# Kernel optimization log

Hardware: AMD Instinct MI355X
Metric: run time of the kernel (lower is better)

The kernel has to match this reference:

```python
import jax, jax.numpy as jnp
import numpy as np

N = 50000          # nodes
E = 800000         # edges (avg degree 16)
IN_C = 3
HEADS = 4
NUM_GRAPHS = 8
NUM_CLASSES = 10


def setup_inputs() -> dict:
    key = jax.random.key(0)
    ks = jax.random.split(key, 12)
    x = jax.random.normal(ks[0], (N, IN_C), jnp.float32)
    edge_index = jax.random.randint(ks[1], (2, E), 0, N, dtype=jnp.int64)
    batch = jnp.sort(jax.random.randint(ks[2], (N,), 0, NUM_GRAPHS, dtype=jnp.int64))

    def glorot(k, shape, fan):
        return jax.random.normal(k, shape, jnp.float32) * np.float32(1.0 / np.sqrt(fan))

    return {
        "x": x, "edge_index": edge_index, "batch": batch,
        "fc0_w": glorot(ks[3], (IN_C, 16), IN_C), "fc0_b": jnp.zeros((16,), jnp.float32),
        "u1": glorot(ks[4], (16, HEADS), 16), "c1": jnp.zeros((HEADS,), jnp.float32),
        "w1": glorot(ks[5], (16, HEADS * 32), 16), "b1": jnp.zeros((32,), jnp.float32),
        "u2": glorot(ks[6], (32, HEADS), 32), "c2": jnp.zeros((HEADS,), jnp.float32),
        "w2": glorot(ks[7], (32, HEADS * 64), 32), "b2": jnp.zeros((64,), jnp.float32),
        "fc1_w": glorot(ks[8], (64, NUM_CLASSES), 64), "fc1_b": jnp.zeros((NUM_CLASSES,), jnp.float32),
    }


def feast_conv(x, src, dst, u, c, w, b, heads, out_c):
    """FeaStConv (t_inv=True): per-edge head softmax on (x_j - x_i), mean aggregation."""
    n = x.shape[0]
    # soft-assignment over heads: [E, H]
    q = jax.nn.softmax((x[src] - x[dst]) @ u + c, axis=-1)
    # transform at node level, then gather per edge: [E, H, out_c]
    xw = (x @ w).reshape(n, heads, out_c)
    msg = jnp.einsum('eh,ehc->ec', q, xw[src])           # [E, out_c]
    agg = jax.ops.segment_sum(msg, dst, num_segments=n)  # sum over incoming edges
    cnt = jax.ops.segment_sum(jnp.ones((src.shape[0],), x.dtype), dst, num_segments=n)
    return agg / jnp.maximum(cnt, 1.0)[:, None] + b


def global_mean_pool(x, batch, num_graphs):
    s = jax.ops.segment_sum(x, batch, num_segments=num_graphs)
    cnt = jax.ops.segment_sum(jnp.ones((x.shape[0],), x.dtype), batch, num_segments=num_graphs)
    return s / jnp.maximum(cnt, 1.0)[:, None]


def reference(x, edge_index, batch, fc0_w, fc0_b, u1, c1, w1, b1, u2, c2, w2, b2, fc1_w, fc1_b):
    src, dst = edge_index[0], edge_index[1]   # x_j = x[src], x_i = x[dst]
    h = jax.nn.relu(x @ fc0_w + fc0_b)                              # [N, 16]
    h = jax.nn.relu(feast_conv(h, src, dst, u1, c1, w1, b1, HEADS, 32))  # [N, 32]
    h = jax.nn.relu(feast_conv(h, src, dst, u2, c2, w2, b2, HEADS, 64))  # [N, 64]
    g = global_mean_pool(h, batch, NUM_GRAPHS)                      # [G, 64]
    # dropout is identity in eval mode
    return g @ fc1_w + fc1_b                                        # [G, num_classes]
```

## Files before the change

### kernel.cpp

```cpp
#include <hip/hip_runtime.h>

#define N_NODES 50000
#define N_EDGES 800000
#define HEADS 4
#define NUM_GRAPHS 8

__global__ __launch_bounds__(256) void hist_kernel(const int* __restrict__ dst,
                                                   int* __restrict__ deg,
                                                   int* __restrict__ off) {
  int e = blockIdx.x * blockDim.x + threadIdx.x;
  if (e < N_EDGES) off[e] = atomicAdd(&deg[dst[e]], 1);
}

__global__ __launch_bounds__(256) void alloc_kernel(const int* __restrict__ deg,
                                                    int* __restrict__ gctr,
                                                    int* __restrict__ rowstart) {
  int i = blockIdx.x * blockDim.x + threadIdx.x;
  int lane = threadIdx.x & 63;
  int d = (i < N_NODES) ? deg[i] : 0;
  int pre = d;
#pragma unroll
  for (int offd = 1; offd < 64; offd <<= 1) {
    int v = __shfl_up(pre, offd, 64);
    if (lane >= offd) pre += v;
  }
  int total = __shfl(pre, 63, 64);
  int base = 0;
  if (lane == 63) base = atomicAdd(gctr, total);
  base = __shfl(base, 63, 64);
  if (i < N_NODES) rowstart[i] = base + pre - d;
}

__global__ __launch_bounds__(256) void scatter_kernel(const int* __restrict__ src,
                                                      const int* __restrict__ dst,
                                                      const int* __restrict__ rowstart,
                                                      const int* __restrict__ off,
                                                      int* __restrict__ src_perm) {
  int e = blockIdx.x * blockDim.x + threadIdx.x;
  if (e >= N_EDGES) return;
  int p = rowstart[dst[e]] + off[e];
  src_perm[p] = src[e];
}

__global__ __launch_bounds__(256) void fc0_kernel(
    const float* __restrict__ x,
    const float* __restrict__ fc0_w, const float* __restrict__ fc0_b,
    const float* __restrict__ u1,
    float* __restrict__ h0, float* __restrict__ P1) {
  __shared__ float sW0[3 * 16];
  __shared__ float sB0[16];
  __shared__ float sU[16 * 4];
  for (int i = threadIdx.x; i < 48; i += blockDim.x) sW0[i] = fc0_w[i];
  for (int i = threadIdx.x; i < 16; i += blockDim.x) sB0[i] = fc0_b[i];
  for (int i = threadIdx.x; i < 64; i += blockDim.x) sU[i] = u1[i];
  __syncthreads();
  int n = blockIdx.x * blockDim.x + threadIdx.x;
  if (n >= N_NODES) return;
  float x0 = x[n * 3 + 0], x1 = x[n * 3 + 1], x2 = x[n * 3 + 2];
  float h[16];
#pragma unroll
  for (int j = 0; j < 16; j++) {
    float v = x0 * sW0[0 * 16 + j] + x1 * sW0[1 * 16 + j] + x2 * sW0[2 * 16 + j] + sB0[j];
    h[j] = fmaxf(v, 0.f);
    h0[(size_t)n * 16 + j] = h[j];
  }
  float p0 = 0.f, p1 = 0.f, p2 = 0.f, p3 = 0.f;
#pragma unroll
  for (int j = 0; j < 16; j++) {
    p0 += h[j] * sU[j * 4 + 0];
    p1 += h[j] * sU[j * 4 + 1];
    p2 += h[j] * sU[j * 4 + 2];
    p3 += h[j] * sU[j * 4 + 3];
  }
  reinterpret_cast<float4*>(P1)[n] = make_float4(p0, p1, p2, p3);
}

__global__ __launch_bounds__(256) void proj2_kernel(
    const float* __restrict__ h1, const float* __restrict__ u2,
    float* __restrict__ P2) {
  __shared__ float sU[32 * 4];
  for (int i = threadIdx.x; i < 128; i += blockDim.x) sU[i] = u2[i];
  __syncthreads();
  int n = blockIdx.x * blockDim.x + threadIdx.x;
  if (n >= N_NODES) return;
  const float4* hr = reinterpret_cast<const float4*>(h1 + (size_t)n * 32);
  float p0 = 0.f, p1 = 0.f, p2 = 0.f, p3 = 0.f;
#pragma unroll
  for (int j4 = 0; j4 < 8; j4++) {
    float4 a = hr[j4];
#pragma unroll
    for (int k = 0; k < 4; k++) {
      float hv = k == 0 ? a.x : k == 1 ? a.y : k == 2 ? a.z : a.w;
      int j = 4 * j4 + k;
      p0 += hv * sU[j * 4 + 0];
      p1 += hv * sU[j * 4 + 1];
      p2 += hv * sU[j * 4 + 2];
      p3 += hv * sU[j * 4 + 3];
    }
  }
  reinterpret_cast<float4*>(P2)[n] = make_float4(p0, p1, p2, p3);
}

__global__ __launch_bounds__(256) void q_kernel(
    const int* __restrict__ rowstart, const int* __restrict__ deg,
    const int* __restrict__ src_perm,
    const float* __restrict__ P, const float* __restrict__ cb,
    float* __restrict__ q_perm) {
  int wid = (blockIdx.x * (blockDim.x >> 6)) + (threadIdx.x >> 6);
  int lane = threadIdx.x & 63;
  if (wid >= N_NODES) return;
  float4 Pd = reinterpret_cast<const float4*>(P)[wid];
  float b0 = cb[0] - Pd.x, b1 = cb[1] - Pd.y, b2 = cb[2] - Pd.z, b3 = cb[3] - Pd.w;
  int e0 = rowstart[wid];
  int d = deg[wid];
  for (int l = lane; l < d; l += 64) {
    int p = e0 + l;
    int s = src_perm[p];
    float4 Ps = reinterpret_cast<const float4*>(P)[s];
    float l0 = Ps.x + b0, l1 = Ps.y + b1, l2 = Ps.z + b2, l3 = Ps.w + b3;
    float m = fmaxf(fmaxf(l0, l1), fmaxf(l2, l3));
    float e0v = __expf(l0 - m), e1v = __expf(l1 - m), e2v = __expf(l2 - m), e3v = __expf(l3 - m);
    float inv = 1.f / (e0v + e1v + e2v + e3v);
    reinterpret_cast<float4*>(q_perm)[p] =
        make_float4(e0v * inv, e1v * inv, e2v * inv, e3v * inv);
  }
}

__global__ __launch_bounds__(256) void agg1_kernel(
    const int* __restrict__ rowstart, const int* __restrict__ deg,
    const int* __restrict__ src_perm, const float* __restrict__ q_perm,
    const float* __restrict__ h0,
    float* __restrict__ A) {
  int wave = threadIdx.x >> 6;
  int lane = threadIdx.x & 63;
  int g = lane >> 4;
  int j = lane & 15;
  int node = blockIdx.x * 4 + wave;
  if (node >= N_NODES) return;
  int e0 = rowstart[node];
  int e1 = e0 + deg[node];
  const float4* q4 = reinterpret_cast<const float4*>(q_perm);
  float a0 = 0.f, a1 = 0.f, a2 = 0.f, a3 = 0.f;
  int p = e0;
  for (; p + 16 <= e1; p += 16) {
    int sA = src_perm[p + 0 + g];
    int sB = src_perm[p + 4 + g];
    int sC = src_perm[p + 8 + g];
    int sD = src_perm[p + 12 + g];
    float4 qA = q4[p + 0 + g];
    float4 qB = q4[p + 4 + g];
    float4 qC = q4[p + 8 + g];
    float4 qD = q4[p + 12 + g];
    float fA = h0[(size_t)sA * 16 + j];
    float fB = h0[(size_t)sB * 16 + j];
    float fC = h0[(size_t)sC * 16 + j];
    float fD = h0[(size_t)sD * 16 + j];
    a0 += qA.x * fA + qB.x * fB + qC.x * fC + qD.x * fD;
    a1 += qA.y * fA + qB.y * fB + qC.y * fC + qD.y * fD;
    a2 += qA.z * fA + qB.z * fB + qC.z * fC + qD.z * fD;
    a3 += qA.w * fA + qB.w * fB + qC.w * fC + qD.w * fD;
  }
  for (; p + 4 <= e1; p += 4) {
    int s = src_perm[p + g];
    float4 q = q4[p + g];
    float f = h0[(size_t)s * 16 + j];
    a0 += q.x * f; a1 += q.y * f; a2 += q.z * f; a3 += q.w * f;
  }
  int rem = e1 - p;
  if (g < rem) {
    int s = src_perm[p + g];
    float4 q = q4[p + g];
    float f = h0[(size_t)s * 16 + j];
    a0 += q.x * f; a1 += q.y * f; a2 += q.z * f; a3 += q.w * f;
  }
  a0 += __shfl_xor(a0, 16, 64); a0 += __shfl_xor(a0, 32, 64);
  a1 += __shfl_xor(a1, 16, 64); a1 += __shfl_xor(a1, 32, 64);
  a2 += __shfl_xor(a2, 16, 64); a2 += __shfl_xor(a2, 32, 64);
  a3 += __shfl_xor(a3, 16, 64); a3 += __shfl_xor(a3, 32, 64);
  float o = (g == 0) ? a0 : (g == 1) ? a1 : (g == 2) ? a2 : a3;
  A[(size_t)node * 64 + lane] = o;
}

__global__ __launch_bounds__(256) void agg2_kernel(
    const int* __restrict__ rowstart, const int* __restrict__ deg,
    const int* __restrict__ src_perm, const float* __restrict__ q_perm,
    const float* __restrict__ h1,
    float* __restrict__ A) {
  int wave = threadIdx.x >> 6;
  int lane = threadIdx.x & 63;
  int g = lane >> 5;
  int j = lane & 31;
  int node = blockIdx.x * 4 + wave;
  if (node >= N_NODES) return;
  int e0 = rowstart[node];
  int e1 = e0 + deg[node];
  const float4* q4 = reinterpret_cast<const float4*>(q_perm);
  float a0 = 0.f, a1 = 0.f, a2 = 0.f, a3 = 0.f;
  int p = e0;
  for (; p + 8 <= e1; p += 8) {
    int sA = src_perm[p + 0 + g];
    int sB = src_perm[p + 2 + g];
    int sC = src_perm[p + 4 + g];
    int sD = src_perm[p + 6 + g];
    float4 qA = q4[p + 0 + g];
    float4 qB = q4[p + 2 + g];
    float4 qC = q4[p + 4 + g];
    float4 qD = q4[p + 6 + g];
    float fA = h1[(size_t)sA * 32 + j];
    float fB = h1[(size_t)sB * 32 + j];
    float fC = h1[(size_t)sC * 32 + j];
    float fD = h1[(size_t)sD * 32 + j];
    a0 += qA.x * fA + qB.x * fB + qC.x * fC + qD.x * fD;
    a1 += qA.y * fA + qB.y * fB + qC.y * fC + qD.y * fD;
    a2 += qA.z * fA + qB.z * fB + qC.z * fC + qD.z * fD;
    a3 += qA.w * fA + qB.w * fB + qC.w * fC + qD.w * fD;
  }
  for (; p + 2 <= e1; p += 2) {
    int s = src_perm[p + g];
    float4 q = q4[p + g];
    float f = h1[(size_t)s * 32 + j];
    a0 += q.x * f; a1 += q.y * f; a2 += q.z * f; a3 += q.w * f;
  }
  int rem = e1 - p;
  if (g < rem) {
    int s = src_perm[p + g];
    float4 q = q4[p + g];
    float f = h1[(size_t)s * 32 + j];
    a0 += q.x * f; a1 += q.y * f; a2 += q.z * f; a3 += q.w * f;
  }
  a0 += __shfl_xor(a0, 32, 64);
  a1 += __shfl_xor(a1, 32, 64);
  a2 += __shfl_xor(a2, 32, 64);
  a3 += __shfl_xor(a3, 32, 64);
  float oa = (g == 0) ? a0 : a1;
  float ob = (g == 0) ? a2 : a3;
  A[(size_t)node * 128 + lane] = oa;
  A[(size_t)node * 128 + 64 + lane] = ob;
}

__global__ __launch_bounds__(256) void gemm1_kernel(
    const int* __restrict__ deg, const float* __restrict__ A,
    const float* __restrict__ w1, const float* __restrict__ b1,
    float* __restrict__ h1) {
  __shared__ float sB[64 * 32];
  for (int i = threadIdx.x; i < 64 * 32; i += 256) {
    int hj = i / 32, c = i % 32;
    sB[i] = w1[(hj % 16) * 128 + (hj / 16) * 32 + c];
  }
  __syncthreads();
  const float4* sB4 = reinterpret_cast<const float4*>(sB);
  int c4 = threadIdx.x & 7;
  int g = threadIdx.x >> 3;
  int n0 = blockIdx.x * 64 + g * 2;
  int n1 = n0 + 1;
  int na = min(n0, N_NODES - 1);
  int nb = min(n1, N_NODES - 1);
  const float4* A0 = reinterpret_cast<const float4*>(A + (size_t)na * 64);
  const float4* A1 = reinterpret_cast<const float4*>(A + (size_t)nb * 64);
  float4 bc = reinterpret_cast<const float4*>(b1)[c4];
  float4 acc0 = {0, 0, 0, 0}, acc1 = {0, 0, 0, 0};
#pragma unroll 2
  for (int k4 = 0; k4 < 16; k4++) {
    float4 a0 = A0[k4];
    float4 a1 = A1[k4];
    float4 w0 = sB4[(4 * k4 + 0) * 8 + c4];
    float4 wv1 = sB4[(4 * k4 + 1) * 8 + c4];
    float4 w2v = sB4[(4 * k4 + 2) * 8 + c4];
    float4 w3 = sB4[(4 * k4 + 3) * 8 + c4];
    acc0.x += a0.x * w0.x + a0.y * wv1.x + a0.z * w2v.x + a0.w * w3.x;
    acc0.y += a0.x * w0.y + a0.y * wv1.y + a0.z * w2v.y + a0.w * w3.y;
    acc0.z += a0.x * w0.z + a0.y * wv1.z + a0.z * w2v.z + a0.w * w3.z;
    acc0.w += a0.x * w0.w + a0.y * wv1.w + a0.z * w2v.w + a0.w * w3.w;
    acc1.x += a1.x * w0.x + a1.y * wv1.x + a1.z * w2v.x + a1.w * w3.x;
    acc1.y += a1.x * w0.y + a1.y * wv1.y + a1.z * w2v.y + a1.w * w3.y;
    acc1.z += a1.x * w0.z + a1.y * wv1.z + a1.z * w2v.z + a1.w * w3.z;
    acc1.w += a1.x * w0.w + a1.y * wv1.w + a1.z * w2v.w + a1.w * w3.w;
  }
  if (n0 < N_NODES) {
    float inv = 1.f / fmaxf((float)deg[n0], 1.f);
    float4 o = {fmaxf(acc0.x * inv + bc.x, 0.f), fmaxf(acc0.y * inv + bc.y, 0.f),
                fmaxf(acc0.z * inv + bc.z, 0.f), fmaxf(acc0.w * inv + bc.w, 0.f)};
    reinterpret_cast<float4*>(h1 + (size_t)n0 * 32)[c4] = o;
  }
  if (n1 < N_NODES) {
    float inv = 1.f / fmaxf((float)deg[n1], 1.f);
    float4 o = {fmaxf(acc1.x * inv + bc.x, 0.f), fmaxf(acc1.y * inv + bc.y, 0.f),
                fmaxf(acc1.z * inv + bc.z, 0.f), fmaxf(acc1.w * inv + bc.w, 0.f)};
    reinterpret_cast<float4*>(h1 + (size_t)n1 * 32)[c4] = o;
  }
}

__global__ __launch_bounds__(256) void gemm2_kernel(
    const int* __restrict__ deg, const float* __restrict__ A,
    const float* __restrict__ w2, const float* __restrict__ b2,
    float* __restrict__ h2) {
  __shared__ float sB[128 * 64];
  for (int i = threadIdx.x; i < 128 * 64; i += 256) {
    int hj = i / 64, c = i % 64;
    sB[i] = w2[(hj % 32) * 256 + (hj / 32) * 64 + c];
  }
  __syncthreads();
  const float4* sB4 = reinterpret_cast<const float4*>(sB);
  int c4 = threadIdx.x & 15;
  int g = threadIdx.x >> 4;
  int n0 = blockIdx.x * 32 + g * 2;
  int n1 = n0 + 1;
  int na = min(n0, N_NODES - 1);
  int nb = min(n1, N_NODES - 1);
  const float4* A0 = reinterpret_cast<const float4*>(A + (size_t)na * 128);
  const float4* A1 = reinterpret_cast<const float4*>(A + (size_t)nb * 128);
  float4 bc = reinterpret_cast<const float4*>(b2)[c4];
  float4 acc0 = {0, 0, 0, 0}, acc1 = {0, 0, 0, 0};
#pragma unroll 2
  for (int k4 = 0; k4 < 32; k4++) {
    float4 a0 = A0[k4];
    float4 a1 = A1[k4];
    float4 w0 = sB4[(4 * k4 + 0) * 16 + c4];
    float4 wv1 = sB4[(4 * k4 + 1) * 16 + c4];
    float4 w2v = sB4[(4 * k4 + 2) * 16 + c4];
    float4 w3 = sB4[(4 * k4 + 3) * 16 + c4];
    acc0.x += a0.x * w0.x + a0.y * wv1.x + a0.z * w2v.x + a0.w * w3.x;
    acc0.y += a0.x * w0.y + a0.y * wv1.y + a0.z * w2v.y + a0.w * w3.y;
    acc0.z += a0.x * w0.z + a0.y * wv1.z + a0.z * w2v.z + a0.w * w3.z;
    acc0.w += a0.x * w0.w + a0.y * wv1.w + a0.z * w2v.w + a0.w * w3.w;
    acc1.x += a1.x * w0.x + a1.y * wv1.x + a1.z * w2v.x + a1.w * w3.x;
    acc1.y += a1.x * w0.y + a1.y * wv1.y + a1.z * w2v.y + a1.w * w3.y;
    acc1.z += a1.x * w0.z + a1.y * wv1.z + a1.z * w2v.z + a1.w * w3.z;
    acc1.w += a1.x * w0.w + a1.y * wv1.w + a1.z * w2v.w + a1.w * w3.w;
  }
  if (n0 < N_NODES) {
    float inv = 1.f / fmaxf((float)deg[n0], 1.f);
    float4 o = {fmaxf(acc0.x * inv + bc.x, 0.f), fmaxf(acc0.y * inv + bc.y, 0.f),
                fmaxf(acc0.z * inv + bc.z, 0.f), fmaxf(acc0.w * inv + bc.w, 0.f)};
    reinterpret_cast<float4*>(h2 + (size_t)n0 * 64)[c4] = o;
  }
  if (n1 < N_NODES) {
    float inv = 1.f / fmaxf((float)deg[n1], 1.f);
    float4 o = {fmaxf(acc1.x * inv + bc.x, 0.f), fmaxf(acc1.y * inv + bc.y, 0.f),
                fmaxf(acc1.z * inv + bc.z, 0.f), fmaxf(acc1.w * inv + bc.w, 0.f)};
    reinterpret_cast<float4*>(h2 + (size_t)n1 * 64)[c4] = o;
  }
}

#define POOL_CHUNK 64
__global__ __launch_bounds__(256) void pool_kernel(
    const float* __restrict__ h2, const int* __restrict__ batch,
    float* __restrict__ gsum, float* __restrict__ gcnt) {
  int grp = threadIdx.x / 64;
  int c = threadIdx.x % 64;
  int n0 = (blockIdx.x * 4 + grp) * POOL_CHUNK;
  int n1 = min(n0 + POOL_CHUNK, N_NODES);
  if (n0 >= N_NODES) return;
  float acc = 0.f;
  float cacc = 0.f;
  int curg = batch[n0];
  for (int n = n0; n < n1; n++) {
    int g = batch[n];
    float v = h2[(size_t)n * 64 + c];
    if (g != curg) {
      atomicAdd(&gsum[curg * 64 + c], acc);
      if (c == 0) atomicAdd(&gcnt[curg], cacc);
      acc = 0.f;
      cacc = 0.f;
      curg = g;
    }
    acc += v;
    cacc += 1.f;
  }
  atomicAdd(&gsum[curg * 64 + c], acc);
  if (c == 0) atomicAdd(&gcnt[curg], cacc);
}

__global__ __launch_bounds__(128) void head_kernel(
    const float* __restrict__ gsum, const float* __restrict__ gcnt,
    const float* __restrict__ fc1_w, const float* __restrict__ fc1_b,
    float* __restrict__ out) {
  int t = threadIdx.x;
  if (t >= NUM_GRAPHS * 10) return;
  int g = t / 10, k = t % 10;
  float inv = 1.f / fmaxf(gcnt[g], 1.f);
  float s = fc1_b[k];
#pragma unroll
  for (int c = 0; c < 64; c++) s += gsum[g * 64 + c] * inv * fc1_w[c * 10 + k];
  out[g * 10 + k] = s;
}

extern "C" void kernel_launch(void* const* d_in, const int* in_sizes, int n_in,
                              void* d_out, int out_size, void* d_ws, size_t ws_size,
                              hipStream_t stream) {
  const float* x = (const float*)d_in[0];
  const int* edge_index = (const int*)d_in[1];
  const int* batch = (const int*)d_in[2];
  const float* fc0_w = (const float*)d_in[3];
  const float* fc0_b = (const float*)d_in[4];
  const float* u1 = (const float*)d_in[5];
  const float* c1 = (const float*)d_in[6];
  const float* w1 = (const float*)d_in[7];
  const float* b1 = (const float*)d_in[8];
  const float* u2 = (const float*)d_in[9];
  const float* c2 = (const float*)d_in[10];
  const float* w2 = (const float*)d_in[11];
  const float* b2 = (const float*)d_in[12];
  const float* fc1_w = (const float*)d_in[13];
  const float* fc1_b = (const float*)d_in[14];
  float* out = (float*)d_out;

  const int* src = edge_index;
  const int* dst = edge_index + N_EDGES;

  char* wsb = (char*)d_ws;
  int* deg = (int*)wsb;
  int* gctr = deg + N_NODES;
  int* rowstart = (int*)wsb + 50004;
  int* off = rowstart + N_NODES;
  int* src_perm = off + N_EDGES;
  float* q_perm = (float*)wsb + 1700004;
  float* h0 = q_perm + (size_t)N_EDGES * 4;
  float* h1 = h0 + (size_t)N_NODES * 16;
  float* h2 = h1 + (size_t)N_NODES * 32;
  float* A = h2 + (size_t)N_NODES * 64;
  float* P1 = A + (size_t)N_NODES * 128;
  float* P2 = P1 + (size_t)N_NODES * 4;
  float* gsum = P2 + (size_t)N_NODES * 4;
  float* gcnt = gsum + NUM_GRAPHS * 64;

  hipMemsetAsync(deg, 0, (N_NODES + 1) * sizeof(int), stream);
  hipMemsetAsync(gsum, 0, (NUM_GRAPHS * 64 + NUM_GRAPHS) * sizeof(float), stream);

  int nblk = (N_NODES + 255) / 256;
  int eblk = (N_EDGES + 255) / 256;
  int wblk = (N_NODES + 3) / 4;

  hist_kernel<<<eblk, 256, 0, stream>>>(dst, deg, off);
  alloc_kernel<<<nblk, 256, 0, stream>>>(deg, gctr, rowstart);
  scatter_kernel<<<eblk, 256, 0, stream>>>(src, dst, rowstart, off, src_perm);

  fc0_kernel<<<nblk, 256, 0, stream>>>(x, fc0_w, fc0_b, u1, h0, P1);

  q_kernel<<<wblk, 256, 0, stream>>>(rowstart, deg, src_perm, P1, c1, q_perm);
  agg1_kernel<<<wblk, 256, 0, stream>>>(rowstart, deg, src_perm, q_perm, h0, A);
  gemm1_kernel<<<(N_NODES + 63) / 64, 256, 0, stream>>>(deg, A, w1, b1, h1);

  proj2_kernel<<<nblk, 256, 0, stream>>>(h1, u2, P2);
  q_kernel<<<wblk, 256, 0, stream>>>(rowstart, deg, src_perm, P2, c2, q_perm);
  agg2_kernel<<<wblk, 256, 0, stream>>>(rowstart, deg, src_perm, q_perm, h1, A);
  gemm2_kernel<<<(N_NODES + 31) / 32, 256, 0, stream>>>(deg, A, w2, b2, h2);

  int pblk = (N_NODES + POOL_CHUNK * 4 - 1) / (POOL_CHUNK * 4);
  pool_kernel<<<pblk, 256, 0, stream>>>(h2, batch, gsum, gcnt);
  head_kernel<<<1, 128, 0, stream>>>(gsum, gcnt, fc1_w, fc1_b, out);
}
```

Measured before the change: 301.8 us.

## Flatten q_kernel to per-edge threads, fuse proj2 into gemm1, merge memsets

The scatter now stores (src,dst) pairs so q_kernel can run one thread per edge instead of one wave per node. That removes lane idling on low-degree nodes, where a 64-lane wave covers only about 16 edges. The proj2 kernel is folded into gemm1's epilogue, which computes P2 from the fresh h1 tile and reduces it with shuffles. The two memsets become one by moving gsum/gcnt next to deg. The cost is doubling the index array bandwidth in the agg kernels (int2 loads reading only .x) and an extra random P[dst] gather per edge.

Measured after the change: 281.7 us. 6.7% less time.

```diff
diff --git a/kernel.cpp b/kernel.cpp
--- a/kernel.cpp
+++ b/kernel.cpp
@@ -35,11 +35,12 @@
                                                       const int* __restrict__ dst,
                                                       const int* __restrict__ rowstart,
                                                       const int* __restrict__ off,
-                                                      int* __restrict__ src_perm) {
+                                                      int2* __restrict__ sd) {
   int e = blockIdx.x * blockDim.x + threadIdx.x;
   if (e >= N_EDGES) return;
-  int p = rowstart[dst[e]] + off[e];
-  src_perm[p] = src[e];
+  int d = dst[e];
+  int p = rowstart[d] + off[e];
+  sd[p] = make_int2(src[e], d);
 }
 
 __global__ __launch_bounds__(256) void fc0_kernel(
@@ -75,60 +76,29 @@
   reinterpret_cast<float4*>(P1)[n] = make_float4(p0, p1, p2, p3);
 }
 
-__global__ __launch_bounds__(256) void proj2_kernel(
-    const float* __restrict__ h1, const float* __restrict__ u2,
-    float* __restrict__ P2) {
-  __shared__ float sU[32 * 4];
-  for (int i = threadIdx.x; i < 128; i += blockDim.x) sU[i] = u2[i];
-  __syncthreads();
-  int n = blockIdx.x * blockDim.x + threadIdx.x;
-  if (n >= N_NODES) return;
-  const float4* hr = reinterpret_cast<const float4*>(h1 + (size_t)n * 32);
-  float p0 = 0.f, p1 = 0.f, p2 = 0.f, p3 = 0.f;
-#pragma unroll
-  for (int j4 = 0; j4 < 8; j4++) {
-    float4 a = hr[j4];
-#pragma unroll
-    for (int k = 0; k < 4; k++) {
-      float hv = k == 0 ? a.x : k == 1 ? a.y : k == 2 ? a.z : a.w;
-      int j = 4 * j4 + k;
-      p0 += hv * sU[j * 4 + 0];
-      p1 += hv * sU[j * 4 + 1];
-      p2 += hv * sU[j * 4 + 2];
-      p3 += hv * sU[j * 4 + 3];
-    }
-  }
-  reinterpret_cast<float4*>(P2)[n] = make_float4(p0, p1, p2, p3);
-}
-
 __global__ __launch_bounds__(256) void q_kernel(
-    const int* __restrict__ rowstart, const int* __restrict__ deg,
-    const int* __restrict__ src_perm,
+    const int2* __restrict__ sd,
     const float* __restrict__ P, const float* __restrict__ cb,
     float* __restrict__ q_perm) {
-  int wid = (blockIdx.x * (blockDim.x >> 6)) + (threadIdx.x >> 6);
-  int lane = threadIdx.x & 63;
-  if (wid >= N_NODES) return;
-  float4 Pd = reinterpret_cast<const float4*>(P)[wid];
-  float b0 = cb[0] - Pd.x, b1 = cb[1] - Pd.y, b2 = cb[2] - Pd.z, b3 = cb[3] - Pd.w;
-  int e0 = rowstart[wid];
-  int d = deg[wid];
-  for (int l = lane; l < d; l += 64) {
-    int p = e0 + l;
-    int s = src_perm[p];
-    float4 Ps = reinterpret_cast<const float4*>(P)[s];
-    float l0 = Ps.x + b0, l1 = Ps.y + b1, l2 = Ps.z + b2, l3 = Ps.w + b3;
-    float m = fmaxf(fmaxf(l0, l1), fmaxf(l2, l3));
-    float e0v = __expf(l0 - m), e1v = __expf(l1 - m), e2v = __expf(l2 - m), e3v = __expf(l3 - m);
-    float inv = 1.f / (e0v + e1v + e2v + e3v);
-    reinterpret_cast<float4*>(q_perm)[p] =
-        make_float4(e0v * inv, e1v * inv, e2v * inv, e3v * inv);
-  }
+  int p = blockIdx.x * blockDim.x + threadIdx.x;
+  if (p >= N_EDGES) return;
+  int2 e = sd[p];
+  float4 Ps = reinterpret_cast<const float4*>(P)[e.x];
+  float4 Pd = reinterpret_cast<const float4*>(P)[e.y];
+  float l0 = Ps.x - Pd.x + cb[0];
+  float l1 = Ps.y - Pd.y + cb[1];
+  float l2 = Ps.z - Pd.z + cb[2];
+  float l3 = Ps.w - Pd.w + cb[3];
+  float m = fmaxf(fmaxf(l0, l1), fmaxf(l2, l3));
+  float e0v = __expf(l0 - m), e1v = __expf(l1 - m), e2v = __expf(l2 - m), e3v = __expf(l3 - m);
+  float inv = 1.f / (e0v + e1v + e2v + e3v);
+  reinterpret_cast<float4*>(q_perm)[p] =
+      make_float4(e0v * inv, e1v * inv, e2v * inv, e3v * inv);
 }
 
 __global__ __launch_bounds__(256) void agg1_kernel(
     const int* __restrict__ rowstart, const int* __restrict__ deg,
-    const int* __restrict__ src_perm, const float* __restrict__ q_perm,
+    const int2* __restrict__ sd, const float* __restrict__ q_perm,
     const float* __restrict__ h0,
     float* __restrict__ A) {
   int wave = threadIdx.x >> 6;
@@ -143,10 +113,10 @@
   float a0 = 0.f, a1 = 0.f, a2 = 0.f, a3 = 0.f;
   int p = e0;
   for (; p + 16 <= e1; p += 16) {
-    int sA = src_perm[p + 0 + g];
-    int sB = src_perm[p + 4 + g];
-    int sC = src_perm[p + 8 + g];
-    int sD = src_perm[p + 12 + g];
+    int sA = sd[p + 0 + g].x;
+    int sB = sd[p + 4 + g].x;
+    int sC = sd[p + 8 + g].x;
+    int sD = sd[p + 12 + g].x;
     float4 qA = q4[p + 0 + g];
     float4 qB = q4[p + 4 + g];
     float4 qC = q4[p + 8 + g];
@@ -161,14 +131,14 @@
     a3 += qA.w * fA + qB.w * fB + qC.w * fC + qD.w * fD;
   }
   for (; p + 4 <= e1; p += 4) {
-    int s = src_perm[p + g];
+    int s = sd[p + g].x;
     float4 q = q4[p + g];
     float f = h0[(size_t)s * 16 + j];
     a0 += q.x * f; a1 += q.y * f; a2 += q.z * f; a3 += q.w * f;
   }
   int rem = e1 - p;
   if (g < rem) {
-    int s = src_perm[p + g];
+    int s = sd[p + g].x;
     float4 q = q4[p + g];
     float f = h0[(size_t)s * 16 + j];
     a0 += q.x * f; a1 += q.y * f; a2 += q.z * f; a3 += q.w * f;
@@ -183,7 +153,7 @@
 
 __global__ __launch_bounds__(256) void agg2_kernel(
     const int* __restrict__ rowstart, const int* __restrict__ deg,
-    const int* __restrict__ src_perm, const float* __restrict__ q_perm,
+    const int2* __restrict__ sd, const float* __restrict__ q_perm,
     const float* __restrict__ h1,
     float* __restrict__ A) {
   int wave = threadIdx.x >> 6;
@@ -198,10 +168,10 @@
   float a0 = 0.f, a1 = 0.f, a2 = 0.f, a3 = 0.f;
   int p = e0;
   for (; p + 8 <= e1; p += 8) {
-    int sA = src_perm[p + 0 + g];
-    int sB = src_perm[p + 2 + g];
-    int sC = src_perm[p + 4 + g];
-    int sD = src_perm[p + 6 + g];
+    int sA = sd[p + 0 + g].x;
+    int sB = sd[p + 2 + g].x;
+    int sC = sd[p + 4 + g].x;
+    int sD = sd[p + 6 + g].x;
     float4 qA = q4[p + 0 + g];
     float4 qB = q4[p + 2 + g];
     float4 qC = q4[p + 4 + g];
@@ -216,14 +186,14 @@
     a3 += qA.w * fA + qB.w * fB + qC.w * fC + qD.w * fD;
   }
   for (; p + 2 <= e1; p += 2) {
-    int s = src_perm[p + g];
+    int s = sd[p + g].x;
     float4 q = q4[p + g];
     float f = h1[(size_t)s * 32 + j];
     a0 += q.x * f; a1 += q.y * f; a2 += q.z * f; a3 += q.w * f;
   }
   int rem = e1 - p;
   if (g < rem) {
-    int s = src_perm[p + g];
+    int s = sd[p + g].x;
     float4 q = q4[p + g];
     float f = h1[(size_t)s * 32 + j];
     a0 += q.x * f; a1 += q.y * f; a2 += q.z * f; a3 += q.w * f;
@@ -241,12 +211,15 @@
 __global__ __launch_bounds__(256) void gemm1_kernel(
     const int* __restrict__ deg, const float* __restrict__ A,
     const float* __restrict__ w1, const float* __restrict__ b1,
-    float* __restrict__ h1) {
+    const float* __restrict__ u2,
+    float* __restrict__ h1, float* __restrict__ P2) {
   __shared__ float sB[64 * 32];
+  __shared__ float sU[32 * 4];
   for (int i = threadIdx.x; i < 64 * 32; i += 256) {
     int hj = i / 32, c = i % 32;
     sB[i] = w1[(hj % 16) * 128 + (hj / 16) * 32 + c];
   }
+  for (int i = threadIdx.x; i < 128; i += 256) sU[i] = u2[i];
   __syncthreads();
   const float4* sB4 = reinterpret_cast<const float4*>(sB);
   int c4 = threadIdx.x & 7;
@@ -276,17 +249,39 @@
     acc1.z += a1.x * w0.z + a1.y * wv1.z + a1.z * w2v.z + a1.w * w3.z;
     acc1.w += a1.x * w0.w + a1.y * wv1.w + a1.z * w2v.w + a1.w * w3.w;
   }
-  if (n0 < N_NODES) {
-    float inv = 1.f / fmaxf((float)deg[n0], 1.f);
-    float4 o = {fmaxf(acc0.x * inv + bc.x, 0.f), fmaxf(acc0.y * inv + bc.y, 0.f),
-                fmaxf(acc0.z * inv + bc.z, 0.f), fmaxf(acc0.w * inv + bc.w, 0.f)};
-    reinterpret_cast<float4*>(h1 + (size_t)n0 * 32)[c4] = o;
-  }
-  if (n1 < N_NODES) {
-    float inv = 1.f / fmaxf((float)deg[n1], 1.f);
-    float4 o = {fmaxf(acc1.x * inv + bc.x, 0.f), fmaxf(acc1.y * inv + bc.y, 0.f),
-                fmaxf(acc1.z * inv + bc.z, 0.f), fmaxf(acc1.w * inv + bc.w, 0.f)};
-    reinterpret_cast<float4*>(h1 + (size_t)n1 * 32)[c4] = o;
+  float inv0 = 1.f / fmaxf((float)deg[na], 1.f);
+  float inv1 = 1.f / fmaxf((float)deg[nb], 1.f);
+  float4 o0 = {fmaxf(acc0.x * inv0 + bc.x, 0.f), fmaxf(acc0.y * inv0 + bc.y, 0.f),
+               fmaxf(acc0.z * inv0 + bc.z, 0.f), fmaxf(acc0.w * inv0 + bc.w, 0.f)};
+  float4 o1 = {fmaxf(acc1.x * inv1 + bc.x, 0.f), fmaxf(acc1.y * inv1 + bc.y, 0.f),
+               fmaxf(acc1.z * inv1 + bc.z, 0.f), fmaxf(acc1.w * inv1 + bc.w, 0.f)};
+  if (n0 < N_NODES) reinterpret_cast<float4*>(h1 + (size_t)n0 * 32)[c4] = o0;
+  if (n1 < N_NODES) reinterpret_cast<float4*>(h1 + (size_t)n1 * 32)[c4] = o1;
+  float pa[4] = {0, 0, 0, 0}, pb[4] = {0, 0, 0, 0};
+#pragma unroll
+  for (int k = 0; k < 4; k++) {
+    int c = 4 * c4 + k;
+    float v0 = k == 0 ? o0.x : k == 1 ? o0.y : k == 2 ? o0.z : o0.w;
+    float v1 = k == 0 ? o1.x : k == 1 ? o1.y : k == 2 ? o1.z : o1.w;
+#pragma unroll
+    for (int hh = 0; hh < 4; hh++) {
+      pa[hh] += v0 * sU[c * 4 + hh];
+      pb[hh] += v1 * sU[c * 4 + hh];
+    }
+  }
+#pragma unroll
+  for (int msk = 1; msk <= 4; msk <<= 1) {
+#pragma unroll
+    for (int hh = 0; hh < 4; hh++) {
+      pa[hh] += __shfl_xor(pa[hh], msk, 64);
+      pb[hh] += __shfl_xor(pb[hh], msk, 64);
+    }
+  }
+  if (c4 == 0) {
+    if (n0 < N_NODES)
+      reinterpret_cast<float4*>(P2)[n0] = make_float4(pa[0], pa[1], pa[2], pa[3]);
+    if (n1 < N_NODES)
+      reinterpret_cast<float4*>(P2)[n1] = make_float4(pb[0], pb[1], pb[2], pb[3]);
   }
 }
 
@@ -411,21 +406,20 @@
   char* wsb = (char*)d_ws;
   int* deg = (int*)wsb;
   int* gctr = deg + N_NODES;
-  int* rowstart = (int*)wsb + 50004;
+  float* gsum = (float*)wsb + 50004;
+  float* gcnt = gsum + NUM_GRAPHS * 64;
+  int* rowstart = (int*)wsb + 50524;
   int* off = rowstart + N_NODES;
-  int* src_perm = off + N_EDGES;
-  float* q_perm = (float*)wsb + 1700004;
+  int2* sd = (int2*)((int*)wsb + 900524);
+  float* q_perm = (float*)wsb + 2500524;
   float* h0 = q_perm + (size_t)N_EDGES * 4;
   float* h1 = h0 + (size_t)N_NODES * 16;
   float* h2 = h1 + (size_t)N_NODES * 32;
   float* A = h2 + (size_t)N_NODES * 64;
   float* P1 = A + (size_t)N_NODES * 128;
   float* P2 = P1 + (size_t)N_NODES * 4;
-  float* gsum = P2 + (size_t)N_NODES * 4;
-  float* gcnt = gsum + NUM_GRAPHS * 64;
-
-  hipMemsetAsync(deg, 0, (N_NODES + 1) * sizeof(int), stream);
-  hipMemsetAsync(gsum, 0, (NUM_GRAPHS * 64 + NUM_GRAPHS) * sizeof(float), stream);
+
+  hipMemsetAsync(d_ws, 0, 50524 * sizeof(int), stream);
 
   int nblk = (N_NODES + 255) / 256;
   int eblk = (N_EDGES + 255) / 256;
@@ -433,17 +427,16 @@
 
   hist_kernel<<<eblk, 256, 0, stream>>>(dst, deg, off);
   alloc_kernel<<<nblk, 256, 0, stream>>>(deg, gctr, rowstart);
-  scatter_kernel<<<eblk, 256, 0, stream>>>(src, dst, rowstart, off, src_perm);
+  scatter_kernel<<<eblk, 256, 0, stream>>>(src, dst, rowstart, off, sd);
 
   fc0_kernel<<<nblk, 256, 0, stream>>>(x, fc0_w, fc0_b, u1, h0, P1);
 
-  q_kernel<<<wblk, 256, 0, stream>>>(rowstart, deg, src_perm, P1, c1, q_perm);
-  agg1_kernel<<<wblk, 256, 0, stream>>>(rowstart, deg, src_perm, q_perm, h0, A);
-  gemm1_kernel<<<(N_NODES + 63) / 64, 256, 0, stream>>>(deg, A, w1, b1, h1);
-
-  proj2_kernel<<<nblk, 256, 0, stream>>>(h1, u2, P2);
-  q_kernel<<<wblk, 256, 0, stream>>>(rowstart, deg, src_perm, P2, c2, q_perm);
-  agg2_kernel<<<wblk, 256, 0, stream>>>(rowstart, deg, src_perm, q_perm, h1, A);
+  q_kernel<<<eblk, 256, 0, stream>>>(sd, P1, c1, q_perm);
+  agg1_kernel<<<wblk, 256, 0, stream>>>(rowstart, deg, sd, q_perm, h0, A);
+  gemm1_kernel<<<(N_NODES + 63) / 64, 256, 0, stream>>>(deg, A, w1, b1, u2, h1, P2);
+
+  q_kernel<<<eblk, 256, 0, stream>>>(sd, P2, c2, q_perm);
+  agg2_kernel<<<wblk, 256, 0, stream>>>(rowstart, deg, sd, q_perm, h1, A);
   gemm2_kernel<<<(N_NODES + 31) / 32, 256, 0, stream>>>(deg, A, w2, b2, h2);
 
   int pblk = (N_NODES + POOL_CHUNK * 4 - 1) / (POOL_CHUNK * 4);
```
